# Performance work log

Hardware: AMD Instinct MI355X
Metric: run time of the kernel (lower is better)

## Reference

```python
import jax, jax.numpy as jnp
import numpy as np

B, S, N, H, W = 2, 8192, 512, 480, 640
NUM_CLASSES = 10
IMG_MEAN = np.array([103.53, 116.28, 123.675], dtype=np.float32)


def _depth_to_cam(p, Rt):
    # DEPTH (x right, y forward, z up) -> CAM (x right, y down, z forward)
    q = p @ Rt.T
    return jnp.stack([q[..., 0], -q[..., 2], q[..., 1]], axis=-1)


def _cam_to_depth(c, Rt):
    q = jnp.stack([c[..., 0], c[..., 2], -c[..., 1]], axis=-1)
    return q @ Rt


def setup_inputs() -> dict:
    key = jax.random.key(0)
    k1, k2, k3, k4, k5, k6 = jax.random.split(key, 6)
    mean = jnp.asarray(IMG_MEAN)
    # normalized image: raw pixel minus per-channel mean (so (img+mean-128)/128 is in [-1,1])
    img = jax.random.uniform(k1, (B, 3, H, W), jnp.float32) * 255.0 - mean[None, :, None, None]
    # seeds in DEPTH coords: x right, y forward (positive depth), z up
    u = jax.random.uniform(k2, (B, S, 3), jnp.float32)
    seeds = jnp.stack([(u[..., 0] - 0.5) * 4.0, u[..., 1] * 4.0 + 1.0, (u[..., 2] - 0.5) * 2.0], axis=-1)
    cx = jax.random.uniform(k3, (B, N), jnp.float32) * (W - 1)
    cy = jax.random.uniform(k4, (B, N), jnp.float32) * (H - 1)
    wh = jax.random.uniform(k5, (B, N, 2), jnp.float32) * 120.0 + 20.0
    l = jnp.clip(cx - wh[..., 0] / 2, 0.0, W - 1.0)
    r = jnp.clip(cx + wh[..., 0] / 2, 0.0, W - 1.0)
    t = jnp.clip(cy - wh[..., 1] / 2, 0.0, H - 1.0)
    b = jnp.clip(cy + wh[..., 1] / 2, 0.0, H - 1.0)
    conf = jax.random.uniform(k6, (B, N), jnp.float32)
    cls = jax.random.randint(jax.random.fold_in(key, 7), (B, N), 0, NUM_CLASSES).astype(jnp.float32)
    bboxes_2d = jnp.stack([l, t, r, b, conf, cls], axis=-1)  # [B,N,6]
    Rt = jnp.broadcast_to(jnp.eye(3, dtype=jnp.float32), (B, 3, 3))
    K = jnp.broadcast_to(
        jnp.array([[530.0, 0.0, W / 2], [0.0, 530.0, H / 2], [0.0, 0.0, 1.0]], jnp.float32), (B, 3, 3))
    return {"img": img, "bboxes_2d": bboxes_2d, "seeds_3d": seeds, "Rt": Rt, "K": K}


def _per_sample(img, bbox, seeds, Rt, K):
    mean = jnp.asarray(IMG_MEAN)
    f_u, f_v = K[0, 0], K[1, 1]
    cam = _depth_to_cam(seeds, Rt)                       # [S,3] seeds in camera frame
    uv = cam @ K.T
    seed_2d = uv[:, :2] / uv[:, 2:3]                     # [S,2] projected seeds
    sx = jnp.clip(seed_2d[:, 0], 0.0, W - 1.0)
    sy = jnp.clip(seed_2d[:, 1], 0.0, H - 1.0)
    idx = jnp.floor(sy).astype(jnp.int32) * W + jnp.floor(sx).astype(jnp.int32)  # flat pixel index
    # texture cue: gather raw pixels at seed locations, renormalized to [-1,1]
    flat = ((img.reshape(3, -1) + mean[:, None]) - 128.0) / 128.0
    txt = flat[:, idx].T                                  # [S,3]
    l, t, r, b, conf, cls = (bbox[:, j] for j in range(6))
    midx = (l + r) * 0.5
    midy = (t + b) * 0.5
    sxe = seed_2d[:, 0:1]
    sye = seed_2d[:, 1:2]
    in_box = (sxe > l) & (sxe < r) & (sye > t) & (sye < b)    # [S,N]
    # semantic cue: scatter conf into class slot == one_hot * conf
    sem = jax.nn.one_hot(cls.astype(jnp.int32), NUM_CLASSES, dtype=jnp.float32) * conf[:, None]  # [N,C]
    du = midx[None, :] - sxe                              # [S,N]
    dv = midy[None, :] - sye
    x3, y3, z3 = cam[:, 0:1], cam[:, 1:2], cam[:, 2:3]
    geo0 = du * (z3 / f_u)
    geo1 = dv * (z3 / f_v)
    geo_xy = _cam_to_depth(jnp.stack([geo0, geo1, jnp.zeros_like(geo0)], axis=-1), Rt)  # [S,N,3]
    seed_depth = seeds[:, 1:2]                            # depth-frame forward axis
    ratio = seed_depth / (seed_depth + geo_xy[..., 1])
    geo_xy = geo_xy * ratio[..., None]
    geo_vec = _cam_to_depth(
        jnp.stack([geo0 + x3, geo1 + y3, jnp.broadcast_to(z3, geo0.shape)], axis=-1), Rt)
    geo_vec = geo_vec / jnp.linalg.norm(geo_vec, axis=-1, keepdims=True)
    geo_cue = jnp.concatenate([geo_xy[..., jnp.array([0, 2])], geo_vec], axis=-1)  # [S,N,5]
    asgn = jnp.argmin(du * du + dv * dv, axis=1)          # nearest-center bbox per seed
    pos_geo = jnp.take_along_axis(geo_cue, asgn[:, None, None], axis=1)[:, 0]      # [S,5]
    pos = jnp.concatenate([sem[asgn], txt, pos_geo], axis=-1)                      # [S,18]
    valid = in_box.sum(axis=1) > 0
    return jnp.where(valid[:, None], pos, 0.0).T          # [18,S]


def reference(img, bboxes_2d, seeds_3d, Rt, K):
    return jax.vmap(_per_sample)(img, bboxes_2d, seeds_3d, Rt, K)  # [B,18,S]
```

## Files before the change

### kernel.cpp

```cpp
#include <hip/hip_runtime.h>
#include <math.h>

#define WID 640
#define HEI 480
#define SEEDS 8192
#define NBOX 512
#define NCLS 10
#define NFEAT 18
#define TPS 16
#define SPB 16

__global__ __launch_bounds__(256) void votefusion_kernel(
    const float* __restrict__ img,
    const float* __restrict__ bb,
    const float* __restrict__ seeds,
    const float* __restrict__ Rt,
    const float* __restrict__ Km,
    float* __restrict__ out)
{
    const int b   = blockIdx.y;
    const int tid = threadIdx.x;
    const int grp = tid / TPS;
    const int t   = tid % TPS;
    const int s   = blockIdx.x * SPB + grp;

    __shared__ float2 s_mid[NBOX];
    __shared__ float4 s_ltrb[NBOX];
    __shared__ float2 s_cc[NBOX];

    const float* bbB = bb + (size_t)b * NBOX * 6;
    for (int j = tid; j < NBOX; j += 256) {
        float l  = bbB[j * 6 + 0];
        float tt = bbB[j * 6 + 1];
        float r  = bbB[j * 6 + 2];
        float bo = bbB[j * 6 + 3];
        s_mid[j]  = make_float2((l + r) * 0.5f, (tt + bo) * 0.5f);
        s_ltrb[j] = make_float4(l, tt, r, bo);
        s_cc[j]   = make_float2(bbB[j * 6 + 4], bbB[j * 6 + 5]);
    }
    __syncthreads();

    const float* R  = Rt + (size_t)b * 9;
    const float* Ko = Km + (size_t)b * 9;
    const float R00 = R[0], R01 = R[1], R02 = R[2];
    const float R10 = R[3], R11 = R[4], R12 = R[5];
    const float R20 = R[6], R21 = R[7], R22 = R[8];
    const float K00 = Ko[0], K01 = Ko[1], K02 = Ko[2];
    const float K10 = Ko[3], K11 = Ko[4], K12 = Ko[5];
    const float K20 = Ko[6], K21 = Ko[7], K22 = Ko[8];

    const float* sp = seeds + ((size_t)b * SEEDS + s) * 3;
    const float s0 = sp[0], s1 = sp[1], s2 = sp[2];
    const float q0 = R00 * s0 + R01 * s1 + R02 * s2;
    const float q1 = R10 * s0 + R11 * s1 + R12 * s2;
    const float q2 = R20 * s0 + R21 * s1 + R22 * s2;
    const float cam0 = q0, cam1 = -q2, cam2 = q1;
    const float uv0 = K00 * cam0 + K01 * cam1 + K02 * cam2;
    const float uv1 = K10 * cam0 + K11 * cam1 + K12 * cam2;
    const float uv2 = K20 * cam0 + K21 * cam1 + K22 * cam2;
    const float sxe = uv0 / uv2;
    const float sye = uv1 / uv2;

    unsigned long long key = 0xFFFFFFFFFFFFFFFFull;
    int any = 0;
    #pragma unroll 4
    for (int i = 0; i < NBOX / TPS; ++i) {
        const int j = i * TPS + t;
        const float2 m  = s_mid[j];
        const float  du = __fsub_rn(m.x, sxe);
        const float  dv = __fsub_rn(m.y, sye);
        const float  d2 = __fadd_rn(__fmul_rn(du, du), __fmul_rn(dv, dv));
        const unsigned long long k =
            ((unsigned long long)__float_as_uint(d2) << 32) | (unsigned)j;
        key = (k < key) ? k : key;
        const float4 bx = s_ltrb[j];
        any |= (sxe > bx.x) & (sxe < bx.z) & (sye > bx.y) & (sye < bx.w);
    }

    #pragma unroll
    for (int m = 1; m < TPS; m <<= 1) {
        const unsigned long long ok = __shfl_xor(key, m);
        key = (ok < key) ? ok : key;
        any |= __shfl_xor(any, m);
    }

    if (t != 0) return;

    const size_t base = (size_t)b * NFEAT * SEEDS + s;
    if (!any) {
        #pragma unroll
        for (int f = 0; f < NFEAT; ++f) out[base + (size_t)f * SEEDS] = 0.0f;
        return;
    }

    const int bi = (int)(unsigned)(key & 0xFFFFFFFFull);

    float outv[NFEAT];
    const float2 cc = s_cc[bi];
    const float conf = cc.x;
    const int   cls  = (int)cc.y;
    #pragma unroll
    for (int f = 0; f < NCLS; ++f) outv[f] = (f == cls) ? conf : 0.0f;

    const float sx = fminf(fmaxf(sxe, 0.0f), (float)(WID - 1));
    const float sy = fminf(fmaxf(sye, 0.0f), (float)(HEI - 1));
    const int ix = (int)floorf(sx);
    const int iy = (int)floorf(sy);
    const int pidx = iy * WID + ix;
    const float* imgB = img + (size_t)b * 3 * HEI * WID;
    outv[10] = (imgB[0 * HEI * WID + pidx] + 103.53f  - 128.0f) * (1.0f / 128.0f);
    outv[11] = (imgB[1 * HEI * WID + pidx] + 116.28f  - 128.0f) * (1.0f / 128.0f);
    outv[12] = (imgB[2 * HEI * WID + pidx] + 123.675f - 128.0f) * (1.0f / 128.0f);

    const float2 mb = s_mid[bi];
    const float du = mb.x - sxe;
    const float dv = mb.y - sye;
    const float x3 = cam0, y3 = cam1, z3 = cam2;
    const float geo0 = du * (z3 / K00);
    const float geo1 = dv * (z3 / K11);

    const float gxy0 = geo0 * R00 - geo1 * R20;
    const float gxy1 = geo0 * R01 - geo1 * R21;
    const float gxy2 = geo0 * R02 - geo1 * R22;
    const float ratio = s1 / (s1 + gxy1);
    outv[13] = gxy0 * ratio;
    outv[14] = gxy2 * ratio;

    const float a0 = geo0 + x3;
    const float a1 = z3;
    const float a2 = -(geo1 + y3);
    float gv0 = a0 * R00 + a1 * R10 + a2 * R20;
    float gv1 = a0 * R01 + a1 * R11 + a2 * R21;
    float gv2 = a0 * R02 + a1 * R12 + a2 * R22;
    const float nrm = sqrtf(gv0 * gv0 + gv1 * gv1 + gv2 * gv2);
    outv[15] = gv0 / nrm;
    outv[16] = gv1 / nrm;
    outv[17] = gv2 / nrm;

    #pragma unroll
    for (int f = 0; f < NFEAT; ++f) out[base + (size_t)f * SEEDS] = outv[f];
}

extern "C" void kernel_launch(void* const* d_in, const int* in_sizes, int n_in,
                              void* d_out, int out_size, void* d_ws, size_t ws_size,
                              hipStream_t stream) {
    const float* img   = (const float*)d_in[0];
    const float* bb    = (const float*)d_in[1];
    const float* seeds = (const float*)d_in[2];
    const float* Rt    = (const float*)d_in[3];
    const float* K     = (const float*)d_in[4];
    float* out = (float*)d_out;

    const int B = in_sizes[1] / (NBOX * 6);
    dim3 grid(SEEDS / SPB, B);
    votefusion_kernel<<<grid, 256, 0, stream>>>(img, bb, seeds, Rt, K, out);
}
```

Measured before the change: 13.47 us.

## Widen per-seed groups to 32 lanes and spread output features across lanes

Each seed is now handled by 32 threads instead of 16, and 8 seeds are processed per block. The in-box flag is reduced with a wavefront ballot instead of shuffles. The epilogue no longer has one lane compute and write all 18 features serially; each of the first 18 lanes computes and writes one feature, so the three image gathers and the output stores run in parallel. Shared memory drops to two float2 arrays, with box midpoints recomputed in the loop and conf/class read straight from global. This removes the serial single-lane tail and the shuffle-based OR, at the cost of extra arithmetic in the hot loop and redundant geometry work across lanes 13-17.

```diff
diff --git a/kernel.cpp b/kernel.cpp
--- a/kernel.cpp
+++ b/kernel.cpp
@@ -3,12 +3,12 @@
 
 #define WID 640
 #define HEI 480
+#define HW (WID * HEI)
 #define SEEDS 8192
 #define NBOX 512
-#define NCLS 10
 #define NFEAT 18
-#define TPS 16
-#define SPB 16
+#define TPS 32
+#define SPB 8
 
 __global__ __launch_bounds__(256) void votefusion_kernel(
     const float* __restrict__ img,
@@ -20,23 +20,20 @@
 {
     const int b   = blockIdx.y;
     const int tid = threadIdx.x;
-    const int grp = tid / TPS;
-    const int t   = tid % TPS;
+    const int grp = tid >> 5;
+    const int t   = tid & 31;
     const int s   = blockIdx.x * SPB + grp;
 
-    __shared__ float2 s_mid[NBOX];
-    __shared__ float4 s_ltrb[NBOX];
-    __shared__ float2 s_cc[NBOX];
+    __shared__ float2 s_lr[NBOX];
+    __shared__ float2 s_tb[NBOX];
 
     const float* bbB = bb + (size_t)b * NBOX * 6;
+    #pragma unroll
     for (int j = tid; j < NBOX; j += 256) {
-        float l  = bbB[j * 6 + 0];
-        float tt = bbB[j * 6 + 1];
-        float r  = bbB[j * 6 + 2];
-        float bo = bbB[j * 6 + 3];
-        s_mid[j]  = make_float2((l + r) * 0.5f, (tt + bo) * 0.5f);
-        s_ltrb[j] = make_float4(l, tt, r, bo);
-        s_cc[j]   = make_float2(bbB[j * 6 + 4], bbB[j * 6 + 5]);
+        const float2 lt = *(const float2*)(bbB + j * 6);
+        const float2 rb = *(const float2*)(bbB + j * 6 + 2);
+        s_lr[j] = make_float2(lt.x, rb.x);
+        s_tb[j] = make_float2(lt.y, rb.y);
     }
     __syncthreads();
 
@@ -66,79 +63,83 @@
     #pragma unroll 4
     for (int i = 0; i < NBOX / TPS; ++i) {
         const int j = i * TPS + t;
-        const float2 m  = s_mid[j];
-        const float  du = __fsub_rn(m.x, sxe);
-        const float  dv = __fsub_rn(m.y, sye);
-        const float  d2 = __fadd_rn(__fmul_rn(du, du), __fmul_rn(dv, dv));
+        const float2 lr = s_lr[j];
+        const float2 tb = s_tb[j];
+        const float midx = __fmul_rn(__fadd_rn(lr.x, lr.y), 0.5f);
+        const float midy = __fmul_rn(__fadd_rn(tb.x, tb.y), 0.5f);
+        const float du = __fsub_rn(midx, sxe);
+        const float dv = __fsub_rn(midy, sye);
+        const float d2 = __fadd_rn(__fmul_rn(du, du), __fmul_rn(dv, dv));
         const unsigned long long k =
             ((unsigned long long)__float_as_uint(d2) << 32) | (unsigned)j;
         key = (k < key) ? k : key;
-        const float4 bx = s_ltrb[j];
-        any |= (sxe > bx.x) & (sxe < bx.z) & (sye > bx.y) & (sye < bx.w);
+        any |= (sxe > lr.x) & (sxe < lr.y) & (sye > tb.x) & (sye < tb.y);
     }
 
     #pragma unroll
     for (int m = 1; m < TPS; m <<= 1) {
         const unsigned long long ok = __shfl_xor(key, m);
         key = (ok < key) ? ok : key;
-        any |= __shfl_xor(any, m);
     }
-
-    if (t != 0) return;
-
-    const size_t base = (size_t)b * NFEAT * SEEDS + s;
-    if (!any) {
-        #pragma unroll
-        for (int f = 0; f < NFEAT; ++f) out[base + (size_t)f * SEEDS] = 0.0f;
-        return;
+    {
+        const unsigned long long bal = __ballot(any != 0);
+        any = ((unsigned)(bal >> (tid & 32)) != 0u);
     }
 
     const int bi = (int)(unsigned)(key & 0xFFFFFFFFull);
 
-    float outv[NFEAT];
-    const float2 cc = s_cc[bi];
-    const float conf = cc.x;
-    const int   cls  = (int)cc.y;
-    #pragma unroll
-    for (int f = 0; f < NCLS; ++f) outv[f] = (f == cls) ? conf : 0.0f;
+    float val = 0.0f;
+    if (any && t < NFEAT) {
+        if (t < 10) {
+            const float conf = bbB[bi * 6 + 4];
+            const int   cls  = (int)bbB[bi * 6 + 5];
+            val = (t == cls) ? conf : 0.0f;
+        } else if (t < 13) {
+            const float sx = fminf(fmaxf(sxe, 0.0f), (float)(WID - 1));
+            const float sy = fminf(fmaxf(sye, 0.0f), (float)(HEI - 1));
+            const int ix = (int)floorf(sx);
+            const int iy = (int)floorf(sy);
+            const int pidx = iy * WID + ix;
+            const float mc = (t == 10) ? 103.53f : (t == 11) ? 116.28f : 123.675f;
+            const float* imgB = img + (size_t)b * 3 * HW;
+            val = ((imgB[(t - 10) * HW + pidx] + mc) - 128.0f) * (1.0f / 128.0f);
+        } else {
+            const float2 lr = s_lr[bi];
+            const float2 tb = s_tb[bi];
+            const float midx = __fmul_rn(__fadd_rn(lr.x, lr.y), 0.5f);
+            const float midy = __fmul_rn(__fadd_rn(tb.x, tb.y), 0.5f);
+            const float du = midx - sxe;
+            const float dv = midy - sye;
+            const float x3 = cam0, y3 = cam1, z3 = cam2;
+            const float geo0 = du * (z3 / K00);
+            const float geo1 = dv * (z3 / K11);
 
-    const float sx = fminf(fmaxf(sxe, 0.0f), (float)(WID - 1));
-    const float sy = fminf(fmaxf(sye, 0.0f), (float)(HEI - 1));
-    const int ix = (int)floorf(sx);
-    const int iy = (int)floorf(sy);
-    const int pidx = iy * WID + ix;
-    const float* imgB = img + (size_t)b * 3 * HEI * WID;
-    outv[10] = (imgB[0 * HEI * WID + pidx] + 103.53f  - 128.0f) * (1.0f / 128.0f);
-    outv[11] = (imgB[1 * HEI * WID + pidx] + 116.28f  - 128.0f) * (1.0f / 128.0f);
-    outv[12] = (imgB[2 * HEI * WID + pidx] + 123.675f - 128.0f) * (1.0f / 128.0f);
+            const float gxy0 = geo0 * R00 - geo1 * R20;
+            const float gxy1 = geo0 * R01 - geo1 * R21;
+            const float gxy2 = geo0 * R02 - geo1 * R22;
+            const float ratio = s1 / (s1 + gxy1);
+            const float gx = gxy0 * ratio;
+            const float gz = gxy2 * ratio;
 
-    const float2 mb = s_mid[bi];
-    const float du = mb.x - sxe;
-    const float dv = mb.y - sye;
-    const float x3 = cam0, y3 = cam1, z3 = cam2;
-    const float geo0 = du * (z3 / K00);
-    const float geo1 = dv * (z3 / K11);
+            const float a0 = geo0 + x3;
+            const float a1 = z3;
+            const float a2 = -(geo1 + y3);
+            const float gv0 = a0 * R00 + a1 * R10 + a2 * R20;
+            const float gv1 = a0 * R01 + a1 * R11 + a2 * R21;
+            const float gv2 = a0 * R02 + a1 * R12 + a2 * R22;
+            const float inr = 1.0f / sqrtf(gv0 * gv0 + gv1 * gv1 + gv2 * gv2);
+            val = (t == 13) ? gx
+                : (t == 14) ? gz
+                : (t == 15) ? gv0 * inr
+                : (t == 16) ? gv1 * inr
+                :             gv2 * inr;
+        }
+    }
 
-    const float gxy0 = geo0 * R00 - geo1 * R20;
-    const float gxy1 = geo0 * R01 - geo1 * R21;
-    const float gxy2 = geo0 * R02 - geo1 * R22;
-    const float ratio = s1 / (s1 + gxy1);
-    outv[13] = gxy0 * ratio;
-    outv[14] = gxy2 * ratio;
-
-    const float a0 = geo0 + x3;
-    const float a1 = z3;
-    const float a2 = -(geo1 + y3);
-    float gv0 = a0 * R00 + a1 * R10 + a2 * R20;
-    float gv1 = a0 * R01 + a1 * R11 + a2 * R21;
-    float gv2 = a0 * R02 + a1 * R12 + a2 * R22;
-    const float nrm = sqrtf(gv0 * gv0 + gv1 * gv1 + gv2 * gv2);
-    outv[15] = gv0 / nrm;
-    outv[16] = gv1 / nrm;
-    outv[17] = gv2 / nrm;
-
-    #pragma unroll
-    for (int f = 0; f < NFEAT; ++f) out[base + (size_t)f * SEEDS] = outv[f];
+    if (t < NFEAT) {
+        const size_t base = (size_t)b * NFEAT * SEEDS + s;
+        out[base + (size_t)t * SEEDS] = val;
+    }
 }
 
 extern "C" void kernel_launch(void* const* d_in, const int* in_sizes, int n_in,
```

Measured after the change: 14.08 us. 4.5% more time.
